# Performance work log

Hardware: AMD Instinct MI355X
Metric: run time of the kernel (lower is better)

Reference implementation:

```python
import jax, jax.numpy as jnp
import numpy as np

B, S, D = 4, 2048, 2048
H = 16
NOPE, ROPE, VD = 128, 64, 128
QK = NOPE + ROPE            # 192 per-head q/k dim
KVR = 512                   # kv_lora_rank
THETA = 10000.0
EPS = 1e-6
SCALE = QK ** -0.5


def _freqs(seq_len, d, theta):
    inv = 1.0 / (theta ** (np.arange(0, d, 2, dtype=np.float64) / d))
    ang = np.outer(np.arange(seq_len, dtype=np.float64), inv)  # [S, d//2]
    return jnp.asarray(np.cos(ang), jnp.float32), jnp.asarray(np.sin(ang), jnp.float32)


def apply_rope(x, cos, sin):
    # x: [B, S, H, d]; cos/sin: [S, d//2]; complex multiply on (even, odd) pairs
    xr = x.reshape(*x.shape[:-1], -1, 2)
    xe, xo = xr[..., 0], xr[..., 1]
    c = cos[None, :, None, :]
    s = sin[None, :, None, :]
    ye = xe * c - xo * s
    yo = xe * s + xo * c
    return jnp.stack([ye, yo], axis=-1).reshape(x.shape)


def rmsnorm(x, w, eps=EPS):
    return x * jax.lax.rsqrt(jnp.mean(x * x, axis=-1, keepdims=True) + eps) * w


def setup_inputs() -> dict:
    key = jax.random.key(0)
    ks = jax.random.split(key, 6)
    sd = 0.02
    x = jax.random.normal(ks[0], (B, S, D), jnp.float32)
    wq = jax.random.normal(ks[1], (H * QK, D), jnp.float32) * sd
    wkv_a = jax.random.normal(ks[2], (KVR + ROPE, D), jnp.float32) * sd
    kv_norm_w = jnp.ones((KVR,), jnp.float32)
    wkv_b = jax.random.normal(ks[3], (H * (NOPE + VD), KVR), jnp.float32) * sd
    wo = jax.random.normal(ks[4], (D, H * VD), jnp.float32) * sd
    cos, sin = _freqs(S, ROPE, THETA)
    return {"x": x, "wq": wq, "wkv_a": wkv_a, "kv_norm_w": kv_norm_w,
            "wkv_b": wkv_b, "wo": wo, "freqs_cos": cos, "freqs_sin": sin}


def reference(x, wq, wkv_a, kv_norm_w, wkv_b, wo, freqs_cos, freqs_sin):
    b, s, _ = x.shape
    # query projection (q_lora_rank == 0 path)
    q = jnp.einsum('bsd,ed->bse', x, wq).reshape(b, s, H, QK)
    q_nope, q_pe = q[..., :NOPE], q[..., NOPE:]
    q_pe = apply_rope(q_pe, freqs_cos, freqs_sin)

    # low-rank KV latent + decoupled rope key
    kv = jnp.einsum('bsd,ed->bse', x, wkv_a)          # [b,s,KVR+ROPE]
    kv_c, k_pe = kv[..., :KVR], kv[..., KVR:]
    k_pe = apply_rope(k_pe[:, :, None, :], freqs_cos, freqs_sin)  # [b,s,1,ROPE]
    kv_c = rmsnorm(kv_c, kv_norm_w)
    kvb = jnp.einsum('bsr,er->bse', kv_c, wkv_b).reshape(b, s, H, NOPE + VD)
    k_nope, v = kvb[..., :NOPE], kvb[..., NOPE:]
    k = jnp.concatenate([k_nope, jnp.broadcast_to(k_pe, (b, s, H, ROPE))], axis=-1)
    q_full = jnp.concatenate([q_nope, q_pe], axis=-1)

    # causal attention
    scores = jnp.einsum('bqhd,bkhd->bhqk', q_full, k) * SCALE
    mask = jnp.triu(jnp.full((s, s), -jnp.inf, jnp.float32), k=1)
    scores = scores + mask[None, None]
    p = jax.nn.softmax(scores, axis=-1)
    out = jnp.einsum('bhqk,bkhd->bqhd', p, v).reshape(b, s, H * VD)
    return jnp.einsum('bse,de->bsd', out, wo)
```

## Files before the change

### kernel.cpp

```cpp
#include <hip/hip_runtime.h>
#include <math.h>

#define BB 4
#define SS 2048
#define DD 2048
#define HH 16
#define NOPE 128
#define ROPE 64
#define VD 128
#define QKD 192
#define KVR 512
#define NP1 3712
#define ROWS (BB*SS)
#define SCL2 0.1041216338380858f

typedef __attribute__((ext_vector_type(8))) short bf16x8;
typedef __attribute__((ext_vector_type(4))) float f32x4;
typedef unsigned short bfu;
typedef __attribute__((address_space(1))) const void GV;
typedef __attribute__((address_space(3))) void LV;

__device__ __forceinline__ float bf2f(unsigned int u) {
    unsigned int i = u << 16; float f; __builtin_memcpy(&f, &i, 4); return f;
}
__device__ __forceinline__ unsigned int f2bf(float f) {
    unsigned int i; __builtin_memcpy(&i, &f, 4);
    return (i + 0x7fffu + ((i >> 16) & 1u)) >> 16;
}
__device__ __forceinline__ unsigned int cvt_pk_bf16(float lo, float hi) {
    unsigned int r;
    asm("v_cvt_pk_bf16_f32 %0, %1, %2" : "=v"(r) : "v"(lo), "v"(hi));
    return r;
}

__global__ void cast_all(const float* __restrict__ x, const float* __restrict__ wq,
                         const float* __restrict__ wa, const float* __restrict__ wb,
                         const float* __restrict__ wo,
                         bfu* __restrict__ dx, bfu* __restrict__ dq,
                         bfu* __restrict__ da, bfu* __restrict__ dkb,
                         bfu* __restrict__ dvb, bfu* __restrict__ dwo) {
    long i = (long)blockIdx.x * 256 + threadIdx.x;
    const float* src; bfu* dst; long off, n_src; float scl = 1.0f;
    if (i < 4194304L)        { src = x;  dst = dx;  off = i;            n_src = 4194304L; }
    else if (i < 5767168L)   { src = wq; dst = dq;  off = i - 4194304L; n_src = 1572864L; scl = SCL2; }
    else if (i < 6094848L)   { src = wa; dst = da;  off = i - 5767168L; n_src = 294912L;  }
    else if (i < 6619136L)   {
        long off2 = i - 6094848L;
        long row = off2 >> 7, c = off2 & 127;
        long h = row >> 8, wi = row & 255;
        bfu* d2 = (wi < 128) ? dkb : dvb;
        long drow = (h << 7) + (wi & 127);
        float4 v = ((const float4*)wb)[off2];
        unsigned int lo = f2bf(v.x) | (f2bf(v.y) << 16);
        unsigned int hi = f2bf(v.z) | (f2bf(v.w) << 16);
        ((uint2*)d2)[drow * 128 + c] = make_uint2(lo, hi);
        return;
    }
    else if (i < 7667712L)   { src = wo; dst = dwo; off = i - 6619136L; n_src = 1048576L; }
    else return;
    unsigned int lo = 0, hi = 0;
    if (off < n_src) {
        float4 v = ((const float4*)src)[off];
        lo = f2bf(v.x * scl) | (f2bf(v.y * scl) << 16);
        hi = f2bf(v.z * scl) | (f2bf(v.w * scl) << 16);
    }
    ((uint2*)dst)[off] = make_uint2(lo, hi);
}

template <int MODE>
__global__ void __launch_bounds__(256)
gemm_bt(const bfu* __restrict__ A, const bfu* __restrict__ Bt,
        void* __restrict__ Cv, bfu* __restrict__ C2, int N, int K) {
    __shared__ __align__(16) char lds[32768];
    char* AsB = lds;
    char* BsB = lds + 16384;
    const int tid  = threadIdx.x;
    const int lane = tid & 63;
    const int wid  = tid >> 6;
    const int wr   = wid >> 1, wc = wid & 1;
    const int nwg  = gridDim.x * gridDim.y;
    const int flat = blockIdx.y * gridDim.x + blockIdx.x;
    const int swz  = (flat & 7) * (nwg >> 3) + (flat >> 3);
    const long m0 = (long)(swz / gridDim.x) * 128;
    const long n0 = (long)(swz % gridDim.x) * 128;

    f32x4 acc[4][4] = {};

    const int lr = lane >> 3;
    const int SB = (lane & 7) << 4;

    for (int k0 = 0; k0 < K; k0 += 64) {
        __syncthreads();
#pragma unroll
        for (int i = 0; i < 4; ++i) {
            int rb = wid * 32 + i * 8;
            int R  = rb + lr;
            int c  = (SB ^ ((R & 7) << 4)) >> 1;
            const bfu* gA = A  + (m0 + R) * (long)K + k0 + c;
            const bfu* gB = Bt + (n0 + R) * (long)K + k0 + c;
            __builtin_amdgcn_global_load_lds((GV*)gA, (LV*)(AsB + rb * 128), 16, 0, 0);
            __builtin_amdgcn_global_load_lds((GV*)gB, (LV*)(BsB + rb * 128), 16, 0, 0);
        }
        __syncthreads();
#pragma unroll
        for (int kk = 0; kk < 2; ++kk) {
            bf16x8 av[4], bv[4];
            const int cb = kk * 64 + ((lane >> 4) << 4);
#pragma unroll
            for (int m = 0; m < 4; ++m) {
                int R = wr * 64 + m * 16 + (lane & 15);
                av[m] = *(const bf16x8*)(AsB + R * 128 + (cb ^ ((R & 7) << 4)));
            }
#pragma unroll
            for (int n = 0; n < 4; ++n) {
                int R = wc * 64 + n * 16 + (lane & 15);
                bv[n] = *(const bf16x8*)(BsB + R * 128 + (cb ^ ((R & 7) << 4)));
            }
#pragma unroll
            for (int m = 0; m < 4; ++m)
#pragma unroll
                for (int n = 0; n < 4; ++n)
                    acc[m][n] = __builtin_amdgcn_mfma_f32_16x16x32_bf16(av[m], bv[n], acc[m][n], 0, 0, 0);
        }
    }

    const int cr = (lane >> 4) << 2;
    const int cc = lane & 15;
#pragma unroll
    for (int m = 0; m < 4; ++m)
#pragma unroll
        for (int n = 0; n < 4; ++n)
#pragma unroll
            for (int r = 0; r < 4; ++r) {
                long row = m0 + wr * 64 + m * 16 + cr + r;
                long col = n0 + wc * 64 + n * 16 + cc;
                float val = acc[m][n][r];
                if (MODE == 1) {
                    ((float*)Cv)[row * N + col] = val;
                } else if (MODE == 2) {
                    long b_ = row >> 11;
                    long s  = row & 2047;
                    long h  = col >> 7;
                    long d  = col & 127;
                    C2[((b_ * HH + h) * SS + s) * (long)QKD + d] = (bfu)f2bf(val);
                } else if (MODE == 3) {
                    long b_ = row >> 11;
                    long s  = row & 2047;
                    if (col < 3072) {
                        unsigned int h = (unsigned int)col / 192u;
                        unsigned int d = (unsigned int)col - h * 192u;
                        ((bfu*)Cv)[((b_ * HH + h) * SS + s) * (long)QKD + d] = (bfu)f2bf(val);
                    } else {
                        C2[row * 640 + (col - 3072)] = (bfu)f2bf(val);
                    }
                } else {
                    long h  = row >> 7;
                    long v  = row & 127;
                    long b_ = col >> 11;
                    long s  = col & 2047;
                    ((bfu*)Cv)[(((b_ * HH + h) * VD) + v) * SS + s] = (bfu)f2bf(val);
                }
            }
}

__global__ void rope_pe_fill(bfu* __restrict__ qr, const bfu* __restrict__ kpe,
                             bfu* __restrict__ kall,
                             const float* __restrict__ fc, const float* __restrict__ fs) {
    long t = (long)blockIdx.x * 256 + threadIdx.x;
    int  ch = (int)(t & 7);
    long r  = t >> 3;
    int  s  = (int)(r & 2047);
    long bh = (r >> 11) & 63;
    long b_ = bh >> 4;
    if (t < 1048576L) {
        bfu* p = qr + (bh * SS + s) * (long)QKD + NOPE + ch * 8;
        bf16x8 v = *(const bf16x8*)p;
        int i0 = ch * 4;
        unsigned int out[4];
#pragma unroll
        for (int k = 0; k < 4; ++k) {
            float e = bf2f((unsigned short)v[2 * k]);
            float o = bf2f((unsigned short)v[2 * k + 1]);
            float c = fc[s * 32 + i0 + k], sn = fs[s * 32 + i0 + k];
            out[k] = cvt_pk_bf16(e * c - o * sn, e * sn + o * c);
        }
        *(uint4*)p = make_uint4(out[0], out[1], out[2], out[3]);
    } else {
        bf16x8 v = *(const bf16x8*)(kpe + (b_ * SS + s) * (long)ROPE + ch * 8);
        *(bf16x8*)(kall + (bh * SS + s) * (long)QKD + NOPE + ch * 8) = v;
    }
}

__global__ void __launch_bounds__(256)
rms_rope_kv(const bfu* __restrict__ kv1, const float* __restrict__ wn,
            bfu* __restrict__ kvc, bfu* __restrict__ kpe,
            const float* __restrict__ fc, const float* __restrict__ fs) {
    const int row = blockIdx.x;
    const int t   = threadIdx.x;
    const int s   = row & (SS - 1);
    const long base = (long)row * 640;
    unsigned int v = *(const unsigned int*)(kv1 + base + 2 * t);
    float a = bf2f(v & 0xffff), c2 = bf2f(v >> 16);
    float ssum = a * a + c2 * c2;
#pragma unroll
    for (int d = 1; d < 64; d <<= 1) ssum += __shfl_xor(ssum, d);
    __shared__ float red[4];
    const int lane = t & 63, w = t >> 6;
    if (lane == 0) red[w] = ssum;
    __syncthreads();
    float tot = red[0] + red[1] + red[2] + red[3];
    float scale = rsqrtf(tot * (1.0f / 512.0f) + 1e-6f);
    float w0 = wn[2 * t], w1 = wn[2 * t + 1];
    unsigned int out = f2bf(a * scale * w0) | (f2bf(c2 * scale * w1) << 16);
    *(unsigned int*)(kvc + (long)row * KVR + 2 * t) = out;
    if (t < 32) {
        unsigned int pv = *(const unsigned int*)(kv1 + base + KVR + 2 * t);
        float e = bf2f(pv & 0xffff), o = bf2f(pv >> 16);
        float cc = fc[s * 32 + t], sn = fs[s * 32 + t];
        unsigned int po = f2bf(e * cc - o * sn) | (f2bf(e * sn + o * cc) << 16);
        *(unsigned int*)(kpe + (long)row * ROPE + 2 * t) = po;
    }
}

template <bool MASKED>
__device__ __forceinline__ void attn_tile64(
    const char* kbuf, const char* vbuf, char* pw,
    const bf16x8 (&qf)[6], f32x4 (&accv)[8],
    float& ms, float& ls, int kv0, int qa, int ql, int kg, int lane) {
    f32x4 sc[4] = {};
#pragma unroll
    for (int j = 0; j < 4; ++j)
#pragma unroll
        for (int d = 0; d < 6; ++d) {
            int row  = j * 16 + ql;
            int slot = (d * 4 + kg) ^ (ql & 7);
            bf16x8 kf = *(const bf16x8*)(kbuf + row * 384 + slot * 16);
            sc[j] = __builtin_amdgcn_mfma_f32_16x16x32_bf16(kf, qf[d], sc[j], 0, 0, 0);
        }
    float p[4][4];
    float mx = -1e30f;
#pragma unroll
    for (int j = 0; j < 4; ++j)
#pragma unroll
        for (int r = 0; r < 4; ++r) {
            float s = sc[j][r];
            if (MASKED) {
                int kv = kv0 + j * 16 + kg * 4 + r;
                s = (kv > qa) ? -1e30f : s;
            }
            p[j][r] = s;
            mx = fmaxf(mx, s);
        }
    mx = fmaxf(mx, __shfl_xor(mx, 16));
    mx = fmaxf(mx, __shfl_xor(mx, 32));
    float rs = 0.f;
    if (__all(mx <= ms)) {
#pragma unroll
        for (int j = 0; j < 4; ++j)
#pragma unroll
            for (int r = 0; r < 4; ++r) {
                float e = exp2f(p[j][r] - ms);
                p[j][r] = e;
                rs += e;
            }
        rs += __shfl_xor(rs, 16);
        rs += __shfl_xor(rs, 32);
        ls += rs;
    } else {
        float mn = fmaxf(ms, mx);
        float al = exp2f(ms - mn);
        ms = mn;
#pragma unroll
        for (int j = 0; j < 4; ++j)
#pragma unroll
            for (int r = 0; r < 4; ++r) {
                float e = exp2f(p[j][r] - mn);
                p[j][r] = e;
                rs += e;
            }
        rs += __shfl_xor(rs, 16);
        rs += __shfl_xor(rs, 32);
        ls = ls * al + rs;
        float alT[4];
#pragma unroll
        for (int r = 0; r < 4; ++r)
            alT[r] = __shfl(al, (lane & 48) + kg * 4 + r);
#pragma unroll
        for (int v8 = 0; v8 < 8; ++v8)
#pragma unroll
            for (int r = 0; r < 4; ++r)
                accv[v8][r] *= alT[r];
    }
#pragma unroll
    for (int j = 0; j < 4; ++j) {
        uint2 u;
        u.x = cvt_pk_bf16(p[j][0], p[j][1]);
        u.y = cvt_pk_bf16(p[j][2], p[j][3]);
        int slot = (2 * j + (kg >> 1)) ^ (ql & 7);
        *(uint2*)(pw + ql * 128 + slot * 16 + (kg & 1) * 8) = u;
    }
    asm volatile("s_waitcnt lgkmcnt(0)" ::: "memory");
#pragma unroll
    for (int t2 = 0; t2 < 2; ++t2) {
        int ps = (t2 * 4 + kg) ^ (ql & 7);
        bf16x8 pa = *(const bf16x8*)(pw + ql * 128 + ps * 16);
#pragma unroll
        for (int v8 = 0; v8 < 8; ++v8) {
            int vrow = v8 * 16 + ql;
            int vs   = (t2 * 4 + kg) ^ (ql & 7);
            bf16x8 vf = *(const bf16x8*)(vbuf + vrow * 128 + vs * 16);
            accv[v8] = __builtin_amdgcn_mfma_f32_16x16x32_bf16(pa, vf, accv[v8], 0, 0, 0);
        }
    }
}

__global__ void __launch_bounds__(512)
attn(const bfu* __restrict__ qr, const bfu* __restrict__ kall,
     const bfu* __restrict__ vt, bfu* __restrict__ ao) {
    __shared__ __align__(16) char kbuf[2][64 * 384];
    __shared__ __align__(16) char vbuf[2][128 * 128];
    __shared__ __align__(16) char pbuf[8][2048];
    const int tid  = threadIdx.x;
    const int lane = tid & 63;
    const int w    = tid >> 6;
    const int ql   = lane & 15;
    const int kg   = lane >> 4;
    const int bid  = blockIdx.x;
    const int qb   = 15 - (bid >> 6);
    const int bh   = bid & 63;
    const int h    = bh & 15;
    const int b    = bh >> 4;
    const char* Q  = (const char*)(qr + (long)bh * SS * QKD);
    const char* Kp = (const char*)(kall + (long)bh * SS * QKD);
    const char* Vp = (const char*)(vt + (long)bh * VD * SS);
    char* pw = pbuf[w];

    const int qa_min = qb * 128 + w * 16;
    const int qa = qa_min + ql;

    const char* ksrc[3]; int kdst[3];
#pragma unroll
    for (int i = 0; i < 3; ++i) {
        int idx  = i * 512 + tid;
        int row  = idx / 24;
        int slot = idx - row * 24;
        int ss   = slot ^ (row & 7);
        ksrc[i]  = Kp + (long)row * 384 + ss * 16;
        kdst[i]  = idx * 16;
    }
    const char* vsrc[2]; int vdst[2];
#pragma unroll
    for (int i = 0; i < 2; ++i) {
        int idx  = i * 512 + tid;
        int row  = idx >> 3;
        int slot = idx & 7;
        int ss   = slot ^ (row & 7);
        vsrc[i]  = Vp + (long)row * (SS * 2) + ss * 16;
        vdst[i]  = idx * 16;
    }
    auto stage = [&](int bi, int kv0) {
        const long ko = (long)kv0 * 384;
        const long vo = (long)kv0 * 2;
#pragma unroll
        for (int i = 0; i < 3; ++i)
            __builtin_amdgcn_global_load_lds((GV*)(ksrc[i] + ko), (LV*)(kbuf[bi] + kdst[i]), 16, 0, 0);
#pragma unroll
        for (int i = 0; i < 2; ++i)
            __builtin_amdgcn_global_load_lds((GV*)(vsrc[i] + vo), (LV*)(vbuf[bi] + vdst[i]), 16, 0, 0);
    };

    bf16x8 qf[6];
#pragma unroll
    for (int d = 0; d < 6; ++d)
        qf[d] = *(const bf16x8*)(Q + (long)(qa_min + ql) * 384 + d * 64 + kg * 16);

    f32x4 accv[8] = {};
    float ms = -1e30f, ls = 0.f;
    const int ntiles = 2 * qb + 2;

    stage(0, 0);
    __syncthreads();

    for (int t = 0; t < ntiles; ++t) {
        const int cur = t & 1;
        const int kv0 = t * 64;
        if (t + 1 < ntiles)
            stage(cur ^ 1, kv0 + 64);
        if (kv0 + 63 <= qa_min)
            attn_tile64<false>(kbuf[cur], vbuf[cur], pw, qf, accv, ms, ls, kv0, qa, ql, kg, lane);
        else if (kv0 <= qa_min + 15)
            attn_tile64<true>(kbuf[cur], vbuf[cur], pw, qf, accv, ms, ls, kv0, qa, ql, kg, lane);
        asm volatile("s_waitcnt vmcnt(0)" ::: "memory");
        __builtin_amdgcn_s_barrier();
        asm volatile("" ::: "memory");
    }
    float li[4];
#pragma unroll
    for (int r = 0; r < 4; ++r)
        li[r] = 1.0f / __shfl(ls, (lane & 48) + kg * 4 + r);
#pragma unroll
    for (int v8 = 0; v8 < 8; ++v8)
#pragma unroll
        for (int r = 0; r < 4; ++r) {
            float o = accv[v8][r] * li[r];
            long row = (long)b * SS + qa_min + kg * 4 + r;
            ao[row * (long)(HH * VD) + h * VD + v8 * 16 + ql] = (bfu)f2bf(o);
        }
}

#define O_XB   0L
#define O_WQ   33554432L
#define O_WA   46137344L
#define O_WKB  48758784L
#define O_WVB  50855936L
#define O_WO   52953088L
#define O_KALL 61341696L
#define O_KV1  111673344L
#define O_QR   122159104L
#define O_KVC  172490752L
#define O_KPE  180879360L
#define O_AO   181927936L
#define WS_NEED 215482368L

extern "C" void kernel_launch(void* const* d_in, const int* in_sizes, int n_in,
                              void* d_out, int out_size, void* d_ws, size_t ws_size,
                              hipStream_t stream) {
    const float* x      = (const float*)d_in[0];
    const float* wq     = (const float*)d_in[1];
    const float* wkv_a  = (const float*)d_in[2];
    const float* kvnw   = (const float*)d_in[3];
    const float* wkv_b  = (const float*)d_in[4];
    const float* wo     = (const float*)d_in[5];
    const float* fcos   = (const float*)d_in[6];
    const float* fsin   = (const float*)d_in[7];
    if (ws_size < (size_t)WS_NEED) return;

    char* ws = (char*)d_ws;
    bfu* xb   = (bfu*)(ws + O_XB);
    bfu* wqb  = (bfu*)(ws + O_WQ);
    bfu* wab  = (bfu*)(ws + O_WA);
    bfu* wkb  = (bfu*)(ws + O_WKB);
    bfu* wvb  = (bfu*)(ws + O_WVB);
    bfu* wob  = (bfu*)(ws + O_WO);
    bfu* kall = (bfu*)(ws + O_KALL);
    bfu* kv1  = (bfu*)(ws + O_KV1);
    bfu* qr   = (bfu*)(ws + O_QR);
    bfu* kvc  = (bfu*)(ws + O_KVC);
    bfu* kpe  = (bfu*)(ws + O_KPE);
    bfu* ao   = (bfu*)(ws + O_AO);
    bfu* vt   = xb;

    cast_all<<<29952, 256, 0, stream>>>(x, wq, wkv_a, wkv_b, wo,
                                        xb, wqb, wab, wkb, wvb, wob);

    gemm_bt<3><<<dim3(29, 64), 256, 0, stream>>>(xb, wqb, qr, kv1, NP1, DD);

    rms_rope_kv<<<ROWS, 256, 0, stream>>>(kv1, kvnw, kvc, kpe, fcos, fsin);

    gemm_bt<2><<<dim3(16, 64), 256, 0, stream>>>(kvc, wkb, nullptr, kall, 2048, KVR);

    gemm_bt<4><<<dim3(64, 16), 256, 0, stream>>>(wvb, kvc, vt, nullptr, 8192, KVR);

    rope_pe_fill<<<8192, 256, 0, stream>>>(qr, kpe, kall, fcos, fsin);

    attn<<<1024, 512, 0, stream>>>(qr, kall, vt, ao);

    gemm_bt<1><<<dim3(16, 64), 256, 0, stream>>>(ao, wob, d_out, nullptr, DD, HH * VD);
}
```

Measured before the change: 513.0 us.

## Add 256x256-tile double-buffered GEMM for Q and output projections

Adds a new 512-thread GEMM kernel with 256x256 tiles, double-buffered direct-to-LDS global loads staged in quarters between MFMA groups, and a workgroup swizzle. The Q projection and the final output projection now use it. The fused Q+KV_a projection is split into a separate Q GEMM and a small KV_a GEMM. The larger tiles raise reuse per loaded byte but use 128KB of LDS and many accumulators, so only one workgroup fits per CU. The grid for the output projection is also small (256 blocks), which may underfill the device.

Measured after the change: 472.8 us. -7.8%, faster.

```diff
diff --git a/kernel.cpp b/kernel.cpp
--- a/kernel.cpp
+++ b/kernel.cpp
@@ -10,7 +10,6 @@
 #define VD 128
 #define QKD 192
 #define KVR 512
-#define NP1 3712
 #define ROWS (BB*SS)
 #define SCL2 0.1041216338380858f
 
@@ -135,30 +134,189 @@
                 long row = m0 + wr * 64 + m * 16 + cr + r;
                 long col = n0 + wc * 64 + n * 16 + cc;
                 float val = acc[m][n][r];
-                if (MODE == 1) {
-                    ((float*)Cv)[row * N + col] = val;
+                if (MODE == 0) {
+                    ((bfu*)Cv)[row * N + col] = (bfu)f2bf(val);
                 } else if (MODE == 2) {
                     long b_ = row >> 11;
                     long s  = row & 2047;
                     long h  = col >> 7;
                     long d  = col & 127;
                     C2[((b_ * HH + h) * SS + s) * (long)QKD + d] = (bfu)f2bf(val);
-                } else if (MODE == 3) {
-                    long b_ = row >> 11;
-                    long s  = row & 2047;
-                    if (col < 3072) {
-                        unsigned int h = (unsigned int)col / 192u;
-                        unsigned int d = (unsigned int)col - h * 192u;
-                        ((bfu*)Cv)[((b_ * HH + h) * SS + s) * (long)QKD + d] = (bfu)f2bf(val);
-                    } else {
-                        C2[row * 640 + (col - 3072)] = (bfu)f2bf(val);
-                    }
                 } else {
                     long h  = row >> 7;
                     long v  = row & 127;
                     long b_ = col >> 11;
                     long s  = col & 2047;
                     ((bfu*)Cv)[(((b_ * HH + h) * VD) + v) * SS + s] = (bfu)f2bf(val);
+                }
+            }
+}
+
+template <int MODE>
+__global__ void __launch_bounds__(512)
+gemm256(const bfu* __restrict__ A, const bfu* __restrict__ Bt,
+        void* __restrict__ Cv, int N, int K) {
+    __shared__ __align__(16) char lds[131072];
+    const int tid  = threadIdx.x;
+    const int lane = tid & 63;
+    const int wid  = tid >> 6;
+    const int wm   = wid >> 2, wn = wid & 3;
+    const int nwg  = gridDim.x * gridDim.y;
+    const int flat = blockIdx.y * gridDim.x + blockIdx.x;
+    const int swz  = (flat & 7) * (nwg >> 3) + (flat >> 3);
+    const long m0 = (long)(swz / gridDim.x) * 256;
+    const long n0 = (long)(swz % gridDim.x) * 256;
+
+    int rowj[2], ssj[2], dstj[2];
+#pragma unroll
+    for (int j = 0; j < 2; ++j) {
+        int idx = j * 512 + tid;
+        rowj[j] = idx >> 3;
+        ssj[j]  = (idx & 7) ^ (rowj[j] & 7);
+        dstj[j] = idx * 16;
+    }
+    const long Kl = K;
+    const bfu* aS[2]; const bfu* bS[2];
+#pragma unroll
+    for (int j = 0; j < 2; ++j) {
+        aS[j] = A  + (m0 + rowj[j]) * Kl + ssj[j] * 8;
+        bS[j] = Bt + (n0 + rowj[j]) * Kl + ssj[j] * 8;
+    }
+    const long hstep = 128 * Kl;
+
+    f32x4 acc[8][4] = {};
+    const int NT = K >> 6;
+
+#pragma unroll
+    for (int h = 0; h < 2; ++h)
+#pragma unroll
+        for (int j = 0; j < 2; ++j) {
+            __builtin_amdgcn_global_load_lds((GV*)(aS[j] + h * hstep),
+                (LV*)(lds + h * 16384 + dstj[j]), 16, 0, 0);
+            __builtin_amdgcn_global_load_lds((GV*)(bS[j] + h * hstep),
+                (LV*)(lds + 65536 + h * 16384 + dstj[j]), 16, 0, 0);
+        }
+    asm volatile("s_waitcnt vmcnt(0)" ::: "memory");
+    __builtin_amdgcn_s_barrier();
+
+    const int k0s = (lane >> 4) ^ (lane & 7);
+    const int k1s = k0s ^ 4;
+    const int aro = wm * 16384 + (lane & 15) * 128;
+    const int bro = (wn >> 1) * 16384 + ((wn & 1) * 64 + (lane & 15)) * 128;
+
+    for (int kt = 0; kt < NT; ++kt) {
+        const int cur = kt & 1;
+        const char* Ab = lds + cur * 32768;
+        const char* Bb = lds + 65536 + cur * 32768;
+        char* An = lds + (cur ^ 1) * 32768;
+        char* Bn = lds + 65536 + (cur ^ 1) * 32768;
+        const long knext = (long)(kt + 1) << 6;
+        const bool more = (kt + 1) < NT;
+
+        const char* a0 = Ab + aro + k0s * 16;
+        const char* a1 = Ab + aro + k1s * 16;
+        const char* b0 = Bb + bro + k0s * 16;
+        const char* b1 = Bb + bro + k1s * 16;
+
+        bf16x8 av[4][2], bv[4][2];
+
+        if (more) {
+#pragma unroll
+            for (int j = 0; j < 2; ++j)
+                __builtin_amdgcn_global_load_lds((GV*)(aS[j] + knext), (LV*)(An + dstj[j]), 16, 0, 0);
+        }
+#pragma unroll
+        for (int mi = 0; mi < 4; ++mi) {
+            av[mi][0] = *(const bf16x8*)(a0 + mi * 2048);
+            av[mi][1] = *(const bf16x8*)(a1 + mi * 2048);
+        }
+#pragma unroll
+        for (int ni = 0; ni < 2; ++ni) {
+            bv[ni][0] = *(const bf16x8*)(b0 + ni * 2048);
+            bv[ni][1] = *(const bf16x8*)(b1 + ni * 2048);
+        }
+#pragma unroll
+        for (int mi = 0; mi < 4; ++mi)
+#pragma unroll
+            for (int ni = 0; ni < 2; ++ni)
+#pragma unroll
+                for (int kk = 0; kk < 2; ++kk)
+                    acc[mi][ni] = __builtin_amdgcn_mfma_f32_16x16x32_bf16(av[mi][kk], bv[ni][kk], acc[mi][ni], 0, 0, 0);
+
+        if (more) {
+#pragma unroll
+            for (int j = 0; j < 2; ++j)
+                __builtin_amdgcn_global_load_lds((GV*)(aS[j] + hstep + knext), (LV*)(An + 16384 + dstj[j]), 16, 0, 0);
+        }
+#pragma unroll
+        for (int ni = 0; ni < 2; ++ni) {
+            bv[2 + ni][0] = *(const bf16x8*)(b0 + (2 + ni) * 2048);
+            bv[2 + ni][1] = *(const bf16x8*)(b1 + (2 + ni) * 2048);
+        }
+#pragma unroll
+        for (int mi = 0; mi < 4; ++mi)
+#pragma unroll
+            for (int ni = 0; ni < 2; ++ni)
+#pragma unroll
+                for (int kk = 0; kk < 2; ++kk)
+                    acc[mi][2 + ni] = __builtin_amdgcn_mfma_f32_16x16x32_bf16(av[mi][kk], bv[2 + ni][kk], acc[mi][2 + ni], 0, 0, 0);
+
+        if (more) {
+#pragma unroll
+            for (int j = 0; j < 2; ++j)
+                __builtin_amdgcn_global_load_lds((GV*)(bS[j] + knext), (LV*)(Bn + dstj[j]), 16, 0, 0);
+        }
+#pragma unroll
+        for (int mi = 0; mi < 4; ++mi) {
+            av[mi][0] = *(const bf16x8*)(a0 + (4 + mi) * 2048);
+            av[mi][1] = *(const bf16x8*)(a1 + (4 + mi) * 2048);
+        }
+#pragma unroll
+        for (int mi = 0; mi < 4; ++mi)
+#pragma unroll
+            for (int ni = 0; ni < 2; ++ni)
+#pragma unroll
+                for (int kk = 0; kk < 2; ++kk)
+                    acc[4 + mi][ni] = __builtin_amdgcn_mfma_f32_16x16x32_bf16(av[mi][kk], bv[ni][kk], acc[4 + mi][ni], 0, 0, 0);
+
+        if (more) {
+#pragma unroll
+            for (int j = 0; j < 2; ++j)
+                __builtin_amdgcn_global_load_lds((GV*)(bS[j] + hstep + knext), (LV*)(Bn + 16384 + dstj[j]), 16, 0, 0);
+        }
+#pragma unroll
+        for (int mi = 0; mi < 4; ++mi)
+#pragma unroll
+            for (int ni = 0; ni < 2; ++ni)
+#pragma unroll
+                for (int kk = 0; kk < 2; ++kk)
+                    acc[4 + mi][2 + ni] = __builtin_amdgcn_mfma_f32_16x16x32_bf16(av[mi][kk], bv[2 + ni][kk], acc[4 + mi][2 + ni], 0, 0, 0);
+
+        if (more) {
+            asm volatile("s_waitcnt vmcnt(0)" ::: "memory");
+            __builtin_amdgcn_s_barrier();
+        }
+    }
+
+    const int cr = (lane >> 4) << 2;
+    const int cc = lane & 15;
+#pragma unroll
+    for (int m = 0; m < 8; ++m)
+#pragma unroll
+        for (int n = 0; n < 4; ++n)
+#pragma unroll
+            for (int r = 0; r < 4; ++r) {
+                long row = m0 + wm * 128 + m * 16 + cr + r;
+                long col = n0 + wn * 64 + n * 16 + cc;
+                float val = acc[m][n][r];
+                if (MODE == 1) {
+                    ((float*)Cv)[row * N + col] = val;
+                } else {
+                    long b_ = row >> 11;
+                    long s  = row & 2047;
+                    unsigned int h = (unsigned int)col / 192u;
+                    unsigned int d = (unsigned int)col - h * 192u;
+                    ((bfu*)Cv)[((b_ * HH + h) * SS + s) * (long)QKD + d] = (bfu)f2bf(val);
                 }
             }
 }
@@ -453,17 +611,18 @@
     cast_all<<<29952, 256, 0, stream>>>(x, wq, wkv_a, wkv_b, wo,
                                         xb, wqb, wab, wkb, wvb, wob);
 
-    gemm_bt<3><<<dim3(29, 64), 256, 0, stream>>>(xb, wqb, qr, kv1, NP1, DD);
+    gemm256<0><<<dim3(12, 32), 512, 0, stream>>>(xb, wqb, qr, 3072, DD);
+
+    gemm_bt<0><<<dim3(5, 64), 256, 0, stream>>>(xb, wab, kv1, nullptr, 640, DD);
 
     rms_rope_kv<<<ROWS, 256, 0, stream>>>(kv1, kvnw, kvc, kpe, fcos, fsin);
 
     gemm_bt<2><<<dim3(16, 64), 256, 0, stream>>>(kvc, wkb, nullptr, kall, 2048, KVR);
-
     gemm_bt<4><<<dim3(64, 16), 256, 0, stream>>>(wvb, kvc, vt, nullptr, 8192, KVR);
 
     rope_pe_fill<<<8192, 256, 0, stream>>>(qr, kpe, kall, fcos, fsin);
 
     attn<<<1024, 512, 0, stream>>>(qr, kall, vt, ao);
 
-    gemm_bt<1><<<dim3(16, 64), 256, 0, stream>>>(ao, wob, d_out, nullptr, DD, HH * VD);
-}
+    gemm256<1><<<dim3(8, 32), 512, 0, stream>>>(ao, wob, d_out, 2048, HH * VD);
+}
```
